# Kernel optimization log

Measured on AMD Instinct MI355X. Metric: run time of the kernel, lower is better.

Reference implementation:

```python
import jax, jax.numpy as jnp
import numpy as np

SEQ, D_IN, D_OUT = 8192, 768, 128


def setup_inputs() -> dict:
    key = jax.random.key(0)
    k1, k2, k3, k4 = jax.random.split(key, 4)
    x = jax.random.normal(k1, (SEQ, D_IN), dtype=jnp.float32)
    # torch nn.Linear weights are stored as [d_out, d_in]
    scale = 1.0 / np.sqrt(D_IN)
    w_query = jax.random.normal(k2, (D_OUT, D_IN), dtype=jnp.float32) * scale
    w_key = jax.random.normal(k3, (D_OUT, D_IN), dtype=jnp.float32) * scale
    w_value = jax.random.normal(k4, (D_OUT, D_IN), dtype=jnp.float32) * scale
    return {"x": x, "w_query": w_query, "w_key": w_key, "w_value": w_value}


def reference(x, w_query, w_key, w_value):
    # Linear with bias=False: y = x @ W.T   (W is [d_out, d_in])
    q = x @ w_query.T                      # [N, d_out]
    k = x @ w_key.T                        # [N, d_out]
    v = x @ w_value.T                      # [N, d_out]
    inv_sqrt_d = 1.0 / jnp.sqrt(jnp.float32(k.shape[-1]))
    scores = (q @ k.T) * inv_sqrt_d        # [N, N] -- fully materialized, as in source
    weights = jax.nn.softmax(scores, axis=-1)
    return weights @ v                     # [N, d_out]
```

## Files before the change

kernel.cpp:

```cpp
#include <hip/hip_runtime.h>
#include <stdint.h>

#define SEQ 8192
#define DIN 768
#define DOUT 128

typedef __attribute__((ext_vector_type(8))) short short8;
typedef __attribute__((ext_vector_type(8))) unsigned short ushort8v;
typedef __attribute__((ext_vector_type(4))) float f32x4;

#define CEXPF (1.4426950408889634f * 0.08838834764831845f)

#if __has_builtin(__builtin_amdgcn_exp2f)
#define EXP2(x) __builtin_amdgcn_exp2f(x)
#else
#define EXP2(x) __builtin_exp2f(x)
#endif

__device__ __forceinline__ unsigned short f2bf(float f) {
  return (unsigned short)((__float_as_uint(f) + 0x8000u) >> 16);
}

__device__ __forceinline__ void gload_lds16(const void* g, void* l) {
  __builtin_amdgcn_global_load_lds(
      (const __attribute__((address_space(1))) void*)g,
      (__attribute__((address_space(3))) void*)l, 16, 0, 0);
}

__global__ void wconv_kernel(const float* __restrict__ wq,
                             const float* __restrict__ wk,
                             const float* __restrict__ wv,
                             unsigned short* __restrict__ Wb) {
  int idx4 = (blockIdx.x * 256 + threadIdx.x) * 4;
  int z = idx4 / (DOUT * DIN);
  int rem = idx4 - z * (DOUT * DIN);
  const float* src = (z == 0) ? wq : (z == 1) ? wk : wv;
  float4 v = *(const float4*)(src + rem);
  float sc = (z == 0) ? CEXPF : 1.0f;
  ushort4 o;
  o.x = f2bf(v.x * sc); o.y = f2bf(v.y * sc);
  o.z = f2bf(v.z * sc); o.w = f2bf(v.w * sc);
  *(ushort4*)(Wb + idx4) = o;
}

__launch_bounds__(256, 3)
__global__ void qkv_kernel(const float* __restrict__ x,
                           const unsigned short* __restrict__ Wb,
                           unsigned short* __restrict__ Qb,
                           unsigned short* __restrict__ Kb,
                           unsigned short* __restrict__ Vtb) {
  __shared__ unsigned short smem[4352];

  const int t    = threadIdx.x;
  const int w    = t >> 6;
  const int lane = t & 63;
  const int g    = lane >> 4;
  const int r    = lane & 15;
  const int z    = blockIdx.y;
  const int m0   = blockIdx.x * 32;
  const unsigned short* Wz = Wb + (size_t)z * DOUT * DIN;

  f32x4 acc[2][2];
#pragma unroll
  for (int i = 0; i < 2; i++)
#pragma unroll
    for (int j = 0; j < 2; j++) acc[i][j] = 0.f;

#pragma unroll 2
  for (int kb = 0; kb < DIN; kb += 32) {
    short8 af[2];
#pragma unroll
    for (int mt = 0; mt < 2; mt++)
      af[mt] = *(const short8*)(Wz + (size_t)(w * 32 + mt * 16 + r) * DIN + kb + g * 8);
    short8 bf[2];
#pragma unroll
    for (int nt = 0; nt < 2; nt++) {
      const float* xp = x + (size_t)(m0 + nt * 16 + r) * DIN + kb + g * 8;
      float4 lo = *(const float4*)xp;
      float4 hi = *(const float4*)(xp + 4);
      short8 b;
      b[0] = (short)f2bf(lo.x); b[1] = (short)f2bf(lo.y);
      b[2] = (short)f2bf(lo.z); b[3] = (short)f2bf(lo.w);
      b[4] = (short)f2bf(hi.x); b[5] = (short)f2bf(hi.y);
      b[6] = (short)f2bf(hi.z); b[7] = (short)f2bf(hi.w);
      bf[nt] = b;
    }
#pragma unroll
    for (int mt = 0; mt < 2; mt++)
#pragma unroll
      for (int nt = 0; nt < 2; nt++)
        acc[mt][nt] = __builtin_amdgcn_mfma_f32_16x16x32_bf16(af[mt], bf[nt], acc[mt][nt], 0, 0, 0);
  }

  if (z < 2) {
    unsigned short* out = (z == 0) ? Qb : Kb;
#pragma unroll
    for (int mt = 0; mt < 2; mt++)
#pragma unroll
      for (int nt = 0; nt < 2; nt++) {
        ushort4 o;
        o.x = f2bf(acc[mt][nt][0]); o.y = f2bf(acc[mt][nt][1]);
        o.z = f2bf(acc[mt][nt][2]); o.w = f2bf(acc[mt][nt][3]);
        *(ushort4*)(out + (size_t)(m0 + nt * 16 + r) * DOUT + w * 32 + mt * 16 + g * 4) = o;
      }
  } else {
    unsigned short* ct = smem;
#pragma unroll
    for (int mt = 0; mt < 2; mt++)
#pragma unroll
      for (int nt = 0; nt < 2; nt++) {
        ushort4 o;
        o.x = f2bf(acc[mt][nt][0]); o.y = f2bf(acc[mt][nt][1]);
        o.z = f2bf(acc[mt][nt][2]); o.w = f2bf(acc[mt][nt][3]);
        *(ushort4*)&ct[(nt * 16 + r) * 136 + w * 32 + mt * 16 + g * 4] = o;
      }
    __syncthreads();
    int col  = t >> 1;
    int half = (t & 1) * 16;
#pragma unroll
    for (int h2 = 0; h2 < 2; h2++) {
      ushort8v a;
#pragma unroll
      for (int i = 0; i < 8; i++) a[i] = ct[(half + h2 * 8 + i) * 136 + col];
      *(ushort8v*)(Vtb + (size_t)col * SEQ + m0 + half + h2 * 8) = a;
    }
  }
}

__launch_bounds__(256, 2)
__global__ void attn_kernel(const unsigned short* __restrict__ Qb,
                            const unsigned short* __restrict__ Kb,
                            const unsigned short* __restrict__ Vtb,
                            float* __restrict__ Opart,
                            float* __restrict__ lpart) {
  __shared__ unsigned char lds[51200];
  unsigned char* Kl = lds;
  unsigned char* Vl = lds + 16384;

  const int t    = threadIdx.x;
  const int wave = t >> 6;
  const int lane = t & 63;
  const int g    = lane >> 4;
  const int r    = lane & 15;
  unsigned short* Pl = (unsigned short*)(lds + 32768 + wave * 4608);

  const int qb = blockIdx.x;
  const int sp = blockIdx.y;
  const int q0 = qb * 128 + wave * 32;
  const int kvbase = sp * 1024;

  auto stageK = [&](int kv0) {
#pragma unroll
    for (int c = 0; c < 4; c++) {
      int idx = (wave * 4 + c) * 64 + lane;
      int krow = idx >> 4, kch = idx & 15;
      gload_lds16(Kb + ((size_t)(kv0 + krow) << 7) + ((kch ^ (krow & 15)) << 3),
                  Kl + ((wave * 4 + c) << 10) + (lane << 4));
    }
  };
  auto stageV = [&](int kv0) {
#pragma unroll
    for (int c = 0; c < 4; c++) {
      int idx = (wave * 4 + c) * 64 + lane;
      int d = idx >> 3, c2 = idx & 7;
      gload_lds16(Vtb + (size_t)d * SEQ + kv0 + ((c2 ^ (d & 7)) << 3),
                  Vl + ((wave * 4 + c) << 10) + (lane << 4));
    }
  };

  short8 qf[2][4];
#pragma unroll
  for (int nt = 0; nt < 2; nt++)
#pragma unroll
    for (int kc = 0; kc < 4; kc++)
      qf[nt][kc] = *(const short8*)(Qb + (size_t)(q0 + nt * 16 + r) * DOUT + kc * 32 + g * 8);

  short8 onesf;
#pragma unroll
  for (int j = 0; j < 8; j++) onesf[j] = (r == 0) ? (short)0x3F80 : (short)0;

  f32x4 oacc[2][8];
  f32x4 lacc[2];
#pragma unroll
  for (int st = 0; st < 2; st++) {
    lacc[st] = 0.f;
#pragma unroll
    for (int n = 0; n < 8; n++) oacc[st][n] = 0.f;
  }

  stageK(kvbase);
  stageV(kvbase);
  asm volatile("s_waitcnt vmcnt(0)" ::: "memory");
  __builtin_amdgcn_s_barrier();
  asm volatile("" ::: "memory");

#pragma unroll 1
  for (int it = 0; it < 16; it++) {
    f32x4 sf[4][2];
#pragma unroll
    for (int mt = 0; mt < 4; mt++)
#pragma unroll
      for (int nt = 0; nt < 2; nt++) sf[mt][nt] = 0.f;
    __builtin_amdgcn_s_setprio(1);
#pragma unroll
    for (int mt = 0; mt < 4; mt++) {
      int row = mt * 16 + r;
#pragma unroll
      for (int kc = 0; kc < 4; kc++) {
        short8 kf = *(const short8*)(Kl + row * 256 + (((kc * 4 + g) ^ (row & 15)) << 4));
        sf[mt][0] = __builtin_amdgcn_mfma_f32_16x16x32_bf16(kf, qf[0][kc], sf[mt][0], 0, 0, 0);
        sf[mt][1] = __builtin_amdgcn_mfma_f32_16x16x32_bf16(kf, qf[1][kc], sf[mt][1], 0, 0, 0);
      }
    }
    __builtin_amdgcn_s_setprio(0);

#pragma unroll
    for (int mt = 0; mt < 4; mt++)
#pragma unroll
      for (int nt = 0; nt < 2; nt++) {
        ushort4 p;
        p.x = f2bf(EXP2(sf[mt][nt][0]));
        p.y = f2bf(EXP2(sf[mt][nt][1]));
        p.z = f2bf(EXP2(sf[mt][nt][2]));
        p.w = f2bf(EXP2(sf[mt][nt][3]));
        *(ushort4*)(Pl + (nt * 16 + r) * 72 + mt * 16 + g * 4) = p;
      }
    short8 pf[2][2];
#pragma unroll
    for (int st = 0; st < 2; st++)
#pragma unroll
      for (int c2 = 0; c2 < 2; c2++)
        pf[st][c2] = *(const short8*)(Pl + (st * 16 + r) * 72 + c2 * 32 + g * 8);

    asm volatile("s_waitcnt vmcnt(0)" ::: "memory");
    __builtin_amdgcn_s_barrier();
    asm volatile("" ::: "memory");
    if (it < 15) stageK(kvbase + (it + 1) * 64);

    __builtin_amdgcn_s_setprio(1);
#pragma unroll
    for (int nt = 0; nt < 8; nt++) {
      int d = nt * 16 + r;
#pragma unroll
      for (int c2 = 0; c2 < 2; c2++) {
        short8 vf = *(const short8*)(Vl + d * 128 + (((c2 * 4 + g) ^ (d & 7)) << 4));
        oacc[0][nt] = __builtin_amdgcn_mfma_f32_16x16x32_bf16(pf[0][c2], vf, oacc[0][nt], 0, 0, 0);
        oacc[1][nt] = __builtin_amdgcn_mfma_f32_16x16x32_bf16(pf[1][c2], vf, oacc[1][nt], 0, 0, 0);
      }
    }
#pragma unroll
    for (int st = 0; st < 2; st++) {
      lacc[st] = __builtin_amdgcn_mfma_f32_16x16x32_bf16(pf[st][0], onesf, lacc[st], 0, 0, 0);
      lacc[st] = __builtin_amdgcn_mfma_f32_16x16x32_bf16(pf[st][1], onesf, lacc[st], 0, 0, 0);
    }
    __builtin_amdgcn_s_setprio(0);

    asm volatile("" ::: "memory");
    __builtin_amdgcn_s_barrier();
    asm volatile("" ::: "memory");
    if (it < 15) {
      stageV(kvbase + (it + 1) * 64);
      asm volatile("s_waitcnt vmcnt(4)" ::: "memory");
      __builtin_amdgcn_s_barrier();
      asm volatile("" ::: "memory");
    }
  }

  const size_t pbase = (size_t)sp * SEQ;
#pragma unroll
  for (int st = 0; st < 2; st++)
#pragma unroll
    for (int rr = 0; rr < 4; rr++) {
      int qrow = q0 + st * 16 + g * 4 + rr;
#pragma unroll
      for (int nt = 0; nt < 8; nt++)
        Opart[(pbase + qrow) * DOUT + nt * 16 + r] = oacc[st][nt][rr];
      if (r == 0) lpart[pbase + qrow] = lacc[st][rr];
    }
}

__global__ void combine_kernel(const float* __restrict__ Opart,
                               const float* __restrict__ lpart,
                               float* __restrict__ out) {
  int idx = blockIdx.x * 256 + threadIdx.x;
  int s   = idx >> 5;
  int d4  = (idx & 31) * 4;
  float L = 0.f;
  f32x4 acc = 0.f;
#pragma unroll
  for (int p = 0; p < 8; p++) {
    L += lpart[p * SEQ + s];
    acc += *(const f32x4*)(Opart + ((size_t)p * SEQ + s) * DOUT + d4);
  }
  f32x4 res = acc * (1.0f / L);
  *(f32x4*)(out + (size_t)s * DOUT + d4) = res;
}

extern "C" void kernel_launch(void* const* d_in, const int* in_sizes, int n_in,
                              void* d_out, int out_size, void* d_ws, size_t ws_size,
                              hipStream_t stream) {
  const float* x  = (const float*)d_in[0];
  const float* wq = (const float*)d_in[1];
  const float* wk = (const float*)d_in[2];
  const float* wv = (const float*)d_in[3];
  float* out = (float*)d_out;

  unsigned short* Qb  = (unsigned short*)d_ws;
  unsigned short* Kb  = Qb + (size_t)SEQ * DOUT;
  unsigned short* Vtb = Kb + (size_t)SEQ * DOUT;
  float* Opart = (float*)(Vtb + (size_t)SEQ * DOUT);
  float* lpart = Opart + (size_t)8 * SEQ * DOUT;
  unsigned short* Wb  = (unsigned short*)Opart;
  if (ws_size < (size_t)(6291456 + 33554432 + 262144)) return;

  wconv_kernel<<<dim3(288), 256, 0, stream>>>(wq, wk, wv, Wb);
  qkv_kernel<<<dim3(256, 3), 256, 0, stream>>>(x, Wb, Qb, Kb, Vtb);
  attn_kernel<<<dim3(64, 8), 256, 0, stream>>>(Qb, Kb, Vtb, Opart, lpart);
  combine_kernel<<<dim3(1024), 256, 0, stream>>>(Opart, lpart, out);
}
```

Baseline: 165.7 us.

## Pre-convert x to bf16 and tile QKV projection through double-buffered LDS

Adds a pass that converts x to bf16 and merges it into the weight-conversion kernel. The QKV projection now uses 128-row tiles whose x and W chunks are staged into double-buffered, XOR-swizzled LDS via global_load_lds. Each wave then computes a 32x128 output block from LDS. This targets the redundant global fp32 loads and per-tile conversions of the old 32-row kernel. In exchange it costs an extra bf16 round trip of x through memory, and the grid shrinks to 192 blocks, which may underfill the GPU.

```diff
diff --git a/kernel.cpp b/kernel.cpp
--- a/kernel.cpp
+++ b/kernel.cpp
@@ -27,102 +27,136 @@
       (__attribute__((address_space(3))) void*)l, 16, 0, 0);
 }
 
-__global__ void wconv_kernel(const float* __restrict__ wq,
-                             const float* __restrict__ wk,
-                             const float* __restrict__ wv,
-                             unsigned short* __restrict__ Wb) {
-  int idx4 = (blockIdx.x * 256 + threadIdx.x) * 4;
-  int z = idx4 / (DOUT * DIN);
-  int rem = idx4 - z * (DOUT * DIN);
-  const float* src = (z == 0) ? wq : (z == 1) ? wk : wv;
-  float4 v = *(const float4*)(src + rem);
-  float sc = (z == 0) ? CEXPF : 1.0f;
-  ushort4 o;
-  o.x = f2bf(v.x * sc); o.y = f2bf(v.y * sc);
-  o.z = f2bf(v.z * sc); o.w = f2bf(v.w * sc);
-  *(ushort4*)(Wb + idx4) = o;
-}
-
-__launch_bounds__(256, 3)
-__global__ void qkv_kernel(const float* __restrict__ x,
+__global__ void conv_kernel(const float* __restrict__ x,
+                            const float* __restrict__ wq,
+                            const float* __restrict__ wk,
+                            const float* __restrict__ wv,
+                            unsigned short* __restrict__ xb,
+                            unsigned short* __restrict__ Wb) {
+  int b = blockIdx.x;
+  if (b < 6144) {
+    int idx4 = (b * 256 + threadIdx.x) * 4;
+    float4 v = *(const float4*)(x + idx4);
+    ushort4 o;
+    o.x = f2bf(v.x); o.y = f2bf(v.y); o.z = f2bf(v.z); o.w = f2bf(v.w);
+    *(ushort4*)(xb + idx4) = o;
+  } else {
+    int idx4 = ((b - 6144) * 256 + threadIdx.x) * 4;
+    int z = idx4 / (DOUT * DIN);
+    int rem = idx4 - z * (DOUT * DIN);
+    const float* src = (z == 0) ? wq : (z == 1) ? wk : wv;
+    float4 v = *(const float4*)(src + rem);
+    float sc = (z == 0) ? CEXPF : 1.0f;
+    ushort4 o;
+    o.x = f2bf(v.x * sc); o.y = f2bf(v.y * sc);
+    o.z = f2bf(v.z * sc); o.w = f2bf(v.w * sc);
+    *(ushort4*)(Wb + idx4) = o;
+  }
+}
+
+__launch_bounds__(256, 2)
+__global__ void qkv_kernel(const unsigned short* __restrict__ xb,
                            const unsigned short* __restrict__ Wb,
                            unsigned short* __restrict__ Qb,
                            unsigned short* __restrict__ Kb,
                            unsigned short* __restrict__ Vtb) {
-  __shared__ unsigned short smem[4352];
+  __shared__ unsigned char lds[65536];
 
   const int t    = threadIdx.x;
-  const int w    = t >> 6;
+  const int wave = t >> 6;
   const int lane = t & 63;
   const int g    = lane >> 4;
   const int r    = lane & 15;
   const int z    = blockIdx.y;
-  const int m0   = blockIdx.x * 32;
+  const int m0   = blockIdx.x * 128;
   const unsigned short* Wz = Wb + (size_t)z * DOUT * DIN;
 
-  f32x4 acc[2][2];
-#pragma unroll
-  for (int i = 0; i < 2; i++)
-#pragma unroll
-    for (int j = 0; j < 2; j++) acc[i][j] = 0.f;
-
-#pragma unroll 2
-  for (int kb = 0; kb < DIN; kb += 32) {
-    short8 af[2];
-#pragma unroll
-    for (int mt = 0; mt < 2; mt++)
-      af[mt] = *(const short8*)(Wz + (size_t)(w * 32 + mt * 16 + r) * DIN + kb + g * 8);
-    short8 bf[2];
-#pragma unroll
-    for (int nt = 0; nt < 2; nt++) {
-      const float* xp = x + (size_t)(m0 + nt * 16 + r) * DIN + kb + g * 8;
-      float4 lo = *(const float4*)xp;
-      float4 hi = *(const float4*)(xp + 4);
-      short8 b;
-      b[0] = (short)f2bf(lo.x); b[1] = (short)f2bf(lo.y);
-      b[2] = (short)f2bf(lo.z); b[3] = (short)f2bf(lo.w);
-      b[4] = (short)f2bf(hi.x); b[5] = (short)f2bf(hi.y);
-      b[6] = (short)f2bf(hi.z); b[7] = (short)f2bf(hi.w);
-      bf[nt] = b;
-    }
-#pragma unroll
-    for (int mt = 0; mt < 2; mt++)
-#pragma unroll
-      for (int nt = 0; nt < 2; nt++)
-        acc[mt][nt] = __builtin_amdgcn_mfma_f32_16x16x32_bf16(af[mt], bf[nt], acc[mt][nt], 0, 0, 0);
+  auto stage = [&](int buf, int kb) {
+    unsigned char* xs = lds + buf * 32768;
+    unsigned char* ws = xs + 16384;
+#pragma unroll
+    for (int c = 0; c < 4; c++) {
+      int ci  = (wave * 4 + c) * 64 + lane;
+      int row = ci >> 3, ch = ci & 7;
+      int sc  = (ch ^ (row & 7)) << 3;
+      gload_lds16(xb + (size_t)(m0 + row) * DIN + kb + sc,
+                  xs + ((wave * 4 + c) << 10) + (lane << 4));
+      gload_lds16(Wz + (size_t)row * DIN + kb + sc,
+                  ws + ((wave * 4 + c) << 10) + (lane << 4));
+    }
+  };
+
+  f32x4 acc[8][2];
+#pragma unroll
+  for (int mt = 0; mt < 8; mt++)
+#pragma unroll
+    for (int nt = 0; nt < 2; nt++) acc[mt][nt] = 0.f;
+
+  stage(0, 0);
+  asm volatile("s_waitcnt vmcnt(0)" ::: "memory");
+  __builtin_amdgcn_s_barrier();
+  asm volatile("" ::: "memory");
+
+#pragma unroll 1
+  for (int s = 0; s < 12; s++) {
+    const int cur = s & 1;
+    if (s < 11) stage(cur ^ 1, (s + 1) * 64);
+    unsigned char* xs = lds + cur * 32768;
+    unsigned char* ws = xs + 16384;
+    __builtin_amdgcn_s_setprio(1);
+#pragma unroll
+    for (int kc = 0; kc < 2; kc++) {
+      short8 bfr[2];
+#pragma unroll
+      for (int nt = 0; nt < 2; nt++) {
+        int row = wave * 32 + nt * 16 + r;
+        bfr[nt] = *(const short8*)(xs + row * 128 + (((kc * 4 + g) ^ (row & 7)) << 4));
+      }
+#pragma unroll
+      for (int mt = 0; mt < 8; mt++) {
+        int oc = mt * 16 + r;
+        short8 afr = *(const short8*)(ws + oc * 128 + (((kc * 4 + g) ^ (oc & 7)) << 4));
+        acc[mt][0] = __builtin_amdgcn_mfma_f32_16x16x32_bf16(afr, bfr[0], acc[mt][0], 0, 0, 0);
+        acc[mt][1] = __builtin_amdgcn_mfma_f32_16x16x32_bf16(afr, bfr[1], acc[mt][1], 0, 0, 0);
+      }
+    }
+    __builtin_amdgcn_s_setprio(0);
+    asm volatile("s_waitcnt vmcnt(0)" ::: "memory");
+    __builtin_amdgcn_s_barrier();
+    asm volatile("" ::: "memory");
   }
 
   if (z < 2) {
     unsigned short* out = (z == 0) ? Qb : Kb;
 #pragma unroll
-    for (int mt = 0; mt < 2; mt++)
+    for (int mt = 0; mt < 8; mt++)
 #pragma unroll
       for (int nt = 0; nt < 2; nt++) {
         ushort4 o;
         o.x = f2bf(acc[mt][nt][0]); o.y = f2bf(acc[mt][nt][1]);
         o.z = f2bf(acc[mt][nt][2]); o.w = f2bf(acc[mt][nt][3]);
-        *(ushort4*)(out + (size_t)(m0 + nt * 16 + r) * DOUT + w * 32 + mt * 16 + g * 4) = o;
+        *(ushort4*)(out + (size_t)(m0 + wave * 32 + nt * 16 + r) * DOUT + mt * 16 + g * 4) = o;
       }
   } else {
-    unsigned short* ct = smem;
-#pragma unroll
-    for (int mt = 0; mt < 2; mt++)
+    unsigned short* ct = (unsigned short*)(lds + wave * 8704);
+#pragma unroll
+    for (int mt = 0; mt < 8; mt++)
 #pragma unroll
       for (int nt = 0; nt < 2; nt++) {
         ushort4 o;
         o.x = f2bf(acc[mt][nt][0]); o.y = f2bf(acc[mt][nt][1]);
         o.z = f2bf(acc[mt][nt][2]); o.w = f2bf(acc[mt][nt][3]);
-        *(ushort4*)&ct[(nt * 16 + r) * 136 + w * 32 + mt * 16 + g * 4] = o;
+        *(ushort4*)&ct[(nt * 16 + r) * 136 + mt * 16 + g * 4] = o;
       }
     __syncthreads();
-    int col  = t >> 1;
-    int half = (t & 1) * 16;
-#pragma unroll
-    for (int h2 = 0; h2 < 2; h2++) {
+#pragma unroll
+    for (int pass = 0; pass < 8; pass++) {
+      int col = pass * 16 + (lane >> 2);
+      int ch  = lane & 3;
       ushort8v a;
 #pragma unroll
-      for (int i = 0; i < 8; i++) a[i] = ct[(half + h2 * 8 + i) * 136 + col];
-      *(ushort8v*)(Vtb + (size_t)col * SEQ + m0 + half + h2 * 8) = a;
+      for (int i = 0; i < 8; i++) a[i] = ct[(ch * 8 + i) * 136 + col];
+      *(ushort8v*)(Vtb + (size_t)col * SEQ + m0 + wave * 32 + ch * 8) = a;
     }
   }
 }
@@ -311,10 +345,11 @@
   float* Opart = (float*)(Vtb + (size_t)SEQ * DOUT);
   float* lpart = Opart + (size_t)8 * SEQ * DOUT;
   unsigned short* Wb  = (unsigned short*)Opart;
+  unsigned short* xb  = Wb + (size_t)3 * DOUT * DIN;
   if (ws_size < (size_t)(6291456 + 33554432 + 262144)) return;
 
-  wconv_kernel<<<dim3(288), 256, 0, stream>>>(wq, wk, wv, Wb);
-  qkv_kernel<<<dim3(256, 3), 256, 0, stream>>>(x, Wb, Qb, Kb, Vtb);
+  conv_kernel<<<dim3(6432), 256, 0, stream>>>(x, wq, wk, wv, xb, Wb);
+  qkv_kernel<<<dim3(64, 3), 256, 0, stream>>>(xb, Wb, Qb, Kb, Vtb);
   attn_kernel<<<dim3(64, 8), 256, 0, stream>>>(Qb, Kb, Vtb, Opart, lpart);
   combine_kernel<<<dim3(1024), 256, 0, stream>>>(Opart, lpart, out);
 }
```

After: 133.0 us. -19.7%, faster.
